# Optimization experiments

Measured on AMD Instinct MI355X. Metric: run time of the kernel, lower is better.

The kernel has to match this reference:

```python
import jax, jax.numpy as jnp
import numpy as np

# IntSoftmax constants (I-BERT)
COEF0 = 0.35815147
COEF1 = 0.96963238 / COEF0
COEF2 = 1.0 / COEF0
X0 = -0.6931          # -ln(2)
CONST = 30
MAX_BIT = 32
OUTPUT_BIT = 8
ACT_BIT = 16          # QuantAct(16)


def floor_ste(x):
    # straight-through floor: forward floor, identity gradient
    return x + jax.lax.stop_gradient(jnp.floor(x) - x)


def setup_inputs() -> dict:
    key = jax.random.key(0)
    x = jax.random.normal(key, (1, 16, 2048, 2048), dtype=jnp.float32)
    # quantization step of the incoming attention scores
    scaling_factor = jnp.ones((1,), dtype=jnp.float32) * (1.0 / 256.0)
    return {"x": x, "scaling_factor": scaling_factor}


def reference(x, scaling_factor):
    sf = scaling_factor  # scalar (shape [1])
    x_int = x / sf
    x_int = x_int - jnp.max(x_int, axis=-1, keepdims=True)

    # ---- int_exp ----
    x0_int = jax.lax.stop_gradient(jnp.floor(X0 / sf))        # no_grad in torch
    x_int = jnp.maximum(x_int, CONST * x0_int)
    q = floor_ste(x_int / x0_int)                              # 0 <= q <= CONST
    r = x_int - x0_int * q
    # ---- int_polynomial ----
    b_int = jax.lax.stop_gradient(jnp.floor(COEF1 / sf))
    c_int = jax.lax.stop_gradient(jnp.floor(COEF2 / (sf * sf)))
    z = (r + b_int) * r + c_int
    exp_sf = COEF0 * sf * sf
    exp_int = jnp.maximum(floor_ste(z * jnp.exp2(CONST - q)), 0.0)
    exp_sf = exp_sf / (2.0 ** CONST)

    # ---- QuantAct(16): per-tensor symmetric requantization ----
    x_real = exp_int * exp_sf
    n = 2.0 ** (ACT_BIT - 1) - 1.0
    x_max = jax.lax.stop_gradient(jnp.maximum(jnp.max(x_real), 0.0))
    act_sf = jax.lax.stop_gradient(x_max / n)
    qv = x_real / act_sf
    exp_int = qv + jax.lax.stop_gradient(
        jnp.clip(jnp.round(qv), -n - 1.0, n) - qv)              # round+clamp STE

    # ---- normalize via bit-shift ----
    exp_int_sum = jnp.sum(exp_int, axis=-1, keepdims=True)
    factor = floor_ste((2.0 ** MAX_BIT) / exp_int_sum)
    exp_int = floor_ste(exp_int * factor / (2.0 ** (MAX_BIT - OUTPUT_BIT)))
    out_sf = 1.0 / (2.0 ** OUTPUT_BIT)
    return exp_int * out_sf
```

## Files before the change

kernel.cpp:

```cpp
#include <hip/hip_runtime.h>


constexpr int COLS    = 2048;
constexpr int THREADS = 256;

__global__ __launch_bounds__(THREADS)
void IntSoftmax_43774306680979_kernel(const float* __restrict__ x,
                                      const float* __restrict__ sfp,
                                      float* __restrict__ out) {
    const int row = blockIdx.x;
    const int tid = threadIdx.x;
    const float sf = sfp[0];

    const float x0_int = floorf(__fdiv_rn(-0.6931f, sf));
    const float b_int  = floorf(__fdiv_rn((float)(0.96963238 / 0.35815147), sf));
    const float c_int  = floorf(__fdiv_rn((float)(1.0 / 0.35815147),
                                          __fmul_rn(sf, sf)));
    float exp_sf = __fmul_rn(__fmul_rn(0.35815147f, sf), sf);
    exp_sf = __fdiv_rn(exp_sf, 1073741824.0f);
    const float clampv = __fmul_rn(30.0f, x0_int);
    const float x_max  = __fmul_rn(floorf(__fmul_rn(c_int, 1073741824.0f)), exp_sf);
    const float act_sf = __fdiv_rn(x_max, 32767.0f);
    const float neg_x0 = -x0_int;

    const unsigned sfb = __float_as_uint(sf);
    const bool sf_pow2 = ((sfb & 0x007fffffu) == 0u) && ((sfb & 0x7f800000u) != 0u);
    const float inv_sf = __fdiv_rn(1.0f, sf);

    const float4* __restrict__ xr =
        reinterpret_cast<const float4*>(x + (size_t)row * COLS);
    float4 a = xr[tid];
    float4 b = xr[tid + THREADS];

    float xi[8] = {a.x, a.y, a.z, a.w, b.x, b.y, b.z, b.w};

    float m = -INFINITY;
    if (sf_pow2) {
#pragma unroll
        for (int i = 0; i < 8; ++i) {
            xi[i] = __fmul_rn(xi[i], inv_sf);
            m = fmaxf(m, xi[i]);
        }
    } else {
#pragma unroll
        for (int i = 0; i < 8; ++i) {
            xi[i] = __fdiv_rn(xi[i], sf);
            m = fmaxf(m, xi[i]);
        }
    }
#pragma unroll
    for (int off = 32; off > 0; off >>= 1)
        m = fmaxf(m, __shfl_xor(m, off, 64));

    __shared__ float smax[4];
    __shared__ float ssum[4];
    if ((tid & 63) == 0) smax[tid >> 6] = m;
    __syncthreads();
    const float rowmax = fmaxf(fmaxf(smax[0], smax[1]), fmaxf(smax[2], smax[3]));

    float s = 0.0f;
#pragma unroll
    for (int i = 0; i < 8; ++i) {
        float t = __fsub_rn(xi[i], rowmax);
        t = fmaxf(t, clampv);
        float q = floorf(__fdiv_rn(t, x0_int));
        float r = fmaf(neg_x0, q, t);
        float z = __fadd_rn(__fmul_rn(__fadd_rn(r, b_int), r), c_int);
        int   qi = (int)q;
        float p = __int_as_float((157 - qi) << 23);
        float ei = fmaxf(floorf(__fmul_rn(z, p)), 0.0f);
        float xreal = __fmul_rn(ei, exp_sf);
        float qv = __fdiv_rn(xreal, act_sf);
        float rq = rintf(qv);
        xi[i] = rq;
        s = __fadd_rn(s, rq);
    }

#pragma unroll
    for (int off = 32; off > 0; off >>= 1)
        s = __fadd_rn(s, __shfl_xor(s, off, 64));
    if ((tid & 63) == 0) ssum[tid >> 6] = s;
    __syncthreads();
    const float sum = __fadd_rn(__fadd_rn(ssum[0], ssum[1]),
                                __fadd_rn(ssum[2], ssum[3]));
    const float factor = floorf(__fdiv_rn(4294967296.0f, sum));

    float o[8];
#pragma unroll
    for (int i = 0; i < 8; ++i) {
        float t = __fmul_rn(__fmul_rn(xi[i], factor), 5.9604644775390625e-8f);
        o[i] = __fmul_rn(floorf(t), 0.00390625f);
    }
    float4* __restrict__ orow = reinterpret_cast<float4*>(out + (size_t)row * COLS);
    orow[tid]           = make_float4(o[0], o[1], o[2], o[3]);
    orow[tid + THREADS] = make_float4(o[4], o[5], o[6], o[7]);
}

extern "C" void kernel_launch(void* const* d_in, const int* in_sizes, int n_in,
                              void* d_out, int out_size, void* d_ws, size_t ws_size,
                              hipStream_t stream) {
    const float* x   = (const float*)d_in[0];
    const float* sfp = (const float*)d_in[1];
    float* out       = (float*)d_out;
    const int rows = in_sizes[0] / COLS;
    IntSoftmax_43774306680979_kernel<<<dim3(rows), dim3(THREADS), 0, stream>>>(
        x, sfp, out);
}
```

Baseline: 435.5 us.

## Map one wavefront per row and use nontemporal vector loads/stores

Each 64-lane wavefront now handles a full 2048-element row, 32 elements per lane, with four rows per block. This drops the shared-memory reductions and both block-wide barriers in favor of wave shuffles only. Loads and stores use nontemporal builtins to avoid cache pollution on this streaming kernel. It raises register pressure to hold 32 values per lane and assumes the row count divides by four.

Measured after the change: 416.0 us. -4.5%, faster.

```diff
diff --git a/kernel.cpp b/kernel.cpp
--- a/kernel.cpp
+++ b/kernel.cpp
@@ -1,15 +1,20 @@
 #include <hip/hip_runtime.h>
 
 
+typedef float f32x4 __attribute__((ext_vector_type(4)));
+
 constexpr int COLS    = 2048;
 constexpr int THREADS = 256;
+constexpr int ROWS_PER_BLOCK = 4;
+constexpr int EPL = 32;
 
 __global__ __launch_bounds__(THREADS)
 void IntSoftmax_43774306680979_kernel(const float* __restrict__ x,
                                       const float* __restrict__ sfp,
                                       float* __restrict__ out) {
-    const int row = blockIdx.x;
-    const int tid = threadIdx.x;
+    const int lane = threadIdx.x & 63;
+    const int wave = threadIdx.x >> 6;
+    const size_t row = (size_t)blockIdx.x * ROWS_PER_BLOCK + wave;
     const float sf = sfp[0];
 
     const float x0_int = floorf(__fdiv_rn(-0.6931f, sf));
@@ -27,23 +32,30 @@
     const bool sf_pow2 = ((sfb & 0x007fffffu) == 0u) && ((sfb & 0x7f800000u) != 0u);
     const float inv_sf = __fdiv_rn(1.0f, sf);
 
-    const float4* __restrict__ xr =
-        reinterpret_cast<const float4*>(x + (size_t)row * COLS);
-    float4 a = xr[tid];
-    float4 b = xr[tid + THREADS];
+    const f32x4* __restrict__ xr =
+        reinterpret_cast<const f32x4*>(x + row * COLS);
+    f32x4 v[8];
+#pragma unroll
+    for (int k = 0; k < 8; ++k)
+        v[k] = __builtin_nontemporal_load(&xr[lane + 64 * k]);
 
-    float xi[8] = {a.x, a.y, a.z, a.w, b.x, b.y, b.z, b.w};
+    float xi[EPL];
+#pragma unroll
+    for (int k = 0; k < 8; ++k) {
+        xi[4 * k + 0] = v[k].x; xi[4 * k + 1] = v[k].y;
+        xi[4 * k + 2] = v[k].z; xi[4 * k + 3] = v[k].w;
+    }
 
     float m = -INFINITY;
     if (sf_pow2) {
 #pragma unroll
-        for (int i = 0; i < 8; ++i) {
+        for (int i = 0; i < EPL; ++i) {
             xi[i] = __fmul_rn(xi[i], inv_sf);
             m = fmaxf(m, xi[i]);
         }
     } else {
 #pragma unroll
-        for (int i = 0; i < 8; ++i) {
+        for (int i = 0; i < EPL; ++i) {
             xi[i] = __fdiv_rn(xi[i], sf);
             m = fmaxf(m, xi[i]);
         }
@@ -51,16 +63,11 @@
 #pragma unroll
     for (int off = 32; off > 0; off >>= 1)
         m = fmaxf(m, __shfl_xor(m, off, 64));
-
-    __shared__ float smax[4];
-    __shared__ float ssum[4];
-    if ((tid & 63) == 0) smax[tid >> 6] = m;
-    __syncthreads();
-    const float rowmax = fmaxf(fmaxf(smax[0], smax[1]), fmaxf(smax[2], smax[3]));
+    const float rowmax = m;
 
     float s = 0.0f;
 #pragma unroll
-    for (int i = 0; i < 8; ++i) {
+    for (int i = 0; i < EPL; ++i) {
         float t = __fsub_rn(xi[i], rowmax);
         t = fmaxf(t, clampv);
         float q = floorf(__fdiv_rn(t, x0_int));
@@ -79,21 +86,20 @@
 #pragma unroll
     for (int off = 32; off > 0; off >>= 1)
         s = __fadd_rn(s, __shfl_xor(s, off, 64));
-    if ((tid & 63) == 0) ssum[tid >> 6] = s;
-    __syncthreads();
-    const float sum = __fadd_rn(__fadd_rn(ssum[0], ssum[1]),
-                                __fadd_rn(ssum[2], ssum[3]));
-    const float factor = floorf(__fdiv_rn(4294967296.0f, sum));
+    const float factor = floorf(__fdiv_rn(4294967296.0f, s));
 
-    float o[8];
+    f32x4* __restrict__ orow = reinterpret_cast<f32x4*>(out + row * COLS);
 #pragma unroll
-    for (int i = 0; i < 8; ++i) {
-        float t = __fmul_rn(__fmul_rn(xi[i], factor), 5.9604644775390625e-8f);
-        o[i] = __fmul_rn(floorf(t), 0.00390625f);
+    for (int k = 0; k < 8; ++k) {
+        f32x4 o;
+#pragma unroll
+        for (int j = 0; j < 4; ++j) {
+            float t = __fmul_rn(__fmul_rn(xi[4 * k + j], factor),
+                                5.9604644775390625e-8f);
+            o[j] = __fmul_rn(floorf(t), 0.00390625f);
+        }
+        __builtin_nontemporal_store(o, &orow[lane + 64 * k]);
     }
-    float4* __restrict__ orow = reinterpret_cast<float4*>(out + (size_t)row * COLS);
-    orow[tid]           = make_float4(o[0], o[1], o[2], o[3]);
-    orow[tid + THREADS] = make_float4(o[4], o[5], o[6], o[7]);
 }
 
 extern "C" void kernel_launch(void* const* d_in, const int* in_sizes, int n_in,
@@ -102,7 +108,8 @@
     const float* x   = (const float*)d_in[0];
     const float* sfp = (const float*)d_in[1];
     float* out       = (float*)d_out;
-    const int rows = in_sizes[0] / COLS;
-    IntSoftmax_43774306680979_kernel<<<dim3(rows), dim3(THREADS), 0, stream>>>(
+    const int rows   = in_sizes[0] / COLS;
+    const int blocks = rows / ROWS_PER_BLOCK;
+    IntSoftmax_43774306680979_kernel<<<dim3(blocks), dim3(THREADS), 0, stream>>>(
         x, sfp, out);
 }
```
